# Performance work log

Measured on AMD Instinct MI355X. Metric: run time of the kernel, lower is better.

## Reference

```python
import math
import jax, jax.numpy as jnp
import numpy as np

B, S, D = 8, 1024, 1024
H, DK = 16, 64
NUM_BUCKETS, MAX_DIST = 32, 128
LN_EPS = 1e-6


def _relative_position_bucket(relative_position, num_buckets=NUM_BUCKETS, max_distance=MAX_DIST):
    # bidirectional (encoder) variant of T5 bucketing
    nb = num_buckets // 2
    rel_buckets = (relative_position > 0).astype(jnp.int32) * nb
    rp = jnp.abs(relative_position)
    max_exact = nb // 2
    is_small = rp < max_exact
    rp_large = max_exact + (
        jnp.log(jnp.maximum(rp, 1).astype(jnp.float32) / max_exact)
        / math.log(max_distance / max_exact)
        * (nb - max_exact)
    ).astype(jnp.int32)
    rp_large = jnp.minimum(rp_large, nb - 1)
    return rel_buckets + jnp.where(is_small, rp, rp_large)


def compute_bias(rel_bias, q_len, k_len):
    ctx = jnp.arange(q_len)[:, None]
    mem = jnp.arange(k_len)[None, :]
    buckets = _relative_position_bucket(mem - ctx)        # [q,k]
    values = rel_bias[buckets]                             # [q,k,H]
    return jnp.transpose(values, (2, 0, 1))[None]          # [1,H,q,k]


def switch_layer_norm(x, w, eps=LN_EPS):
    # T5-style: no mean subtraction, no bias
    var = jnp.mean(jnp.square(x.astype(jnp.float32)), axis=-1, keepdims=True)
    return w * (x * jax.lax.rsqrt(var + eps)).astype(x.dtype)


def setup_inputs() -> dict:
    key = jax.random.key(0)
    ks = jax.random.split(key, 6)
    scale = 1.0 / math.sqrt(D)
    return {
        "hidden_states": jax.random.normal(ks[0], (B, S, D), jnp.float32),
        "ln_weight": jnp.ones((D,), jnp.float32),
        "wq": jax.random.normal(ks[1], (D, H * DK), jnp.float32) * scale,
        "wk": jax.random.normal(ks[2], (D, H * DK), jnp.float32) * scale,
        "wv": jax.random.normal(ks[3], (D, H * DK), jnp.float32) * scale,
        "wo": jax.random.normal(ks[4], (H * DK, D), jnp.float32) * scale,
        "rel_bias": jax.random.normal(ks[5], (NUM_BUCKETS, H), jnp.float32),
    }


def reference(hidden_states, ln_weight, wq, wk, wv, wo, rel_bias):
    b, s, d = hidden_states.shape
    normed = switch_layer_norm(hidden_states, ln_weight)
    # projections -> [B,H,S,DK]; T5 applies NO 1/sqrt(dk) scaling
    q = (normed @ wq).reshape(b, s, H, DK).transpose(0, 2, 1, 3)
    k = (normed @ wk).reshape(b, s, H, DK).transpose(0, 2, 1, 3)
    v = (normed @ wv).reshape(b, s, H, DK).transpose(0, 2, 1, 3)
    scores = jnp.einsum("bhqd,bhkd->bhqk", q, k)
    scores = scores + compute_bias(rel_bias, s, s)
    attn = jax.nn.softmax(scores, axis=-1)
    ctx = jnp.einsum("bhqk,bhkd->bhqd", attn, v)
    ctx = ctx.transpose(0, 2, 1, 3).reshape(b, s, H * DK)
    attn_out = ctx @ wo
    return hidden_states + attn_out  # residual of SwitchLayerSelfAttention (dropout=0)
```

## Files before the change

kernel.cpp:

```cpp
#include <hip/hip_runtime.h>

typedef unsigned short u16;
typedef unsigned int u32;
typedef unsigned long long u64;
typedef __attribute__((ext_vector_type(8))) short bf16x8;
typedef __attribute__((ext_vector_type(4))) float f32x4;

__device__ __forceinline__ float bf2f(u16 u) {
  union { u32 i; float f; } c; c.i = ((u32)u) << 16; return c.f;
}
__device__ __forceinline__ u16 f2bf(float f) {
  union { float f; u32 i; } c; c.f = f;
  u32 i = c.i;
  return (u16)((i + 0x7fffu + ((i >> 16) & 1u)) >> 16);
}
__device__ __forceinline__ u32 pkbf(float a, float b) {
  union { float f; u32 i; } ca, cb; ca.f = a; cb.f = b;
  return __builtin_amdgcn_perm(cb.i + 0x8000u, ca.i + 0x8000u, 0x07060302u);
}
__device__ __forceinline__ void async16(const void* g, void* l) {
  __builtin_amdgcn_global_load_lds((const __attribute__((address_space(1))) void*)g,
                                   (__attribute__((address_space(3))) void*)l, 16, 0, 0);
}

__global__ __launch_bounds__(256) void detect_kernel(const u32* __restrict__ X,
                                                     int* __restrict__ flag) {
  __shared__ int part[4];
  const int tid = threadIdx.x, lane = tid & 63, wave = tid >> 6;
  int votes = 0;
  for (int i = tid; i < 4096; i += 256) {
    const u32 u = X[i];
    union { u32 i; float f; } c; c.i = u;
    const float a = fabsf(c.f);
    if (u == 0u || (a > 1e-6f && a < 1e6f)) votes++;
  }
  #pragma unroll
  for (int off = 32; off >= 1; off >>= 1) votes += __shfl_xor(votes, off);
  if (lane == 0) part[wave] = votes;
  __syncthreads();
  if (tid == 0) {
    const int tot = part[0] + part[1] + part[2] + part[3];
    *flag = (tot >= 2048) ? 0 : 1;
  }
}

__global__ __launch_bounds__(256) void prep_kernel(
    const void* __restrict__ W0, const void* __restrict__ W1, const void* __restrict__ W2,
    const void* __restrict__ W3, u16* __restrict__ T0, u16* __restrict__ T1,
    u16* __restrict__ T2, u16* __restrict__ T3, const void* __restrict__ rel_bias,
    float* __restrict__ Tb, const int* __restrict__ flagp) {
  const int f32m = (*flagp == 0);
  const int z = blockIdx.z;
  if (z == 4) {
    const int flat = blockIdx.y * 16 + blockIdx.x;
    const int idx = flat * 256 + threadIdx.x;
    if (idx >= 16 * 2047) return;
    const int h = idx / 2047;
    const int d = idx % 2047 - 1023;
    const int rb = (d > 0) ? 16 : 0;
    const int rp = d < 0 ? -d : d;
    int val;
    if (rp < 8) {
      val = rp;
    } else {
      float t = (logf((float)rp * 0.125f) / 2.772588722239781f) * 8.0f;
      val = 8 + (int)t;
      if (val > 15) val = 15;
    }
    const int bi = (rb + val) * 16 + h;
    Tb[idx] = f32m ? ((const float*)rel_bias)[bi] : bf2f(((const u16*)rel_bias)[bi]);
    return;
  }
  const void* W = (z == 0) ? W0 : (z == 1) ? W1 : (z == 2) ? W2 : W3;
  u16* WT = (z == 0) ? T0 : (z == 1) ? T1 : (z == 2) ? T2 : T3;
  __shared__ u16 t[64][65];
  const int tid = threadIdx.x;
  const int tx = tid & 63, ty = tid >> 6;
  const int n0 = blockIdx.x * 64, k0 = blockIdx.y * 64;
  #pragma unroll
  for (int r = ty; r < 64; r += 4) {
    const size_t idx = (size_t)(k0 + r) * 1024 + n0 + tx;
    t[r][tx] = f32m ? f2bf(((const float*)W)[idx]) : ((const u16*)W)[idx];
  }
  __syncthreads();
  #pragma unroll
  for (int r = ty; r < 64; r += 4) WT[(size_t)(n0 + r) * 1024 + k0 + tx] = t[tx][r];
}

__global__ __launch_bounds__(256) void rmsnorm_kernel(const void* __restrict__ X,
                                                      const void* __restrict__ W,
                                                      u16* __restrict__ Out,
                                                      const int* __restrict__ flagp) {
  const int f32m = (*flagp == 0);
  __shared__ float part[4];
  const int tid = threadIdx.x, lane = tid & 63, wave = tid >> 6;
  const size_t row = blockIdx.x;
  const int c = tid * 4;
  float x0, x1, x2, x3, w0f, w1f, w2f, w3f;
  if (f32m) {
    const float4 xx = *(const float4*)((const float*)X + row * 1024 + c);
    x0 = xx.x; x1 = xx.y; x2 = xx.z; x3 = xx.w;
    const float4 ww = *(const float4*)((const float*)W + c);
    w0f = ww.x; w1f = ww.y; w2f = ww.z; w3f = ww.w;
  } else {
    const u32* px = (const u32*)((const u16*)X + row * 1024 + c);
    const u32 a0 = px[0], a1 = px[1];
    x0 = bf2f((u16)a0); x1 = bf2f((u16)(a0 >> 16));
    x2 = bf2f((u16)a1); x3 = bf2f((u16)(a1 >> 16));
    const u32* pw = (const u32*)((const u16*)W + c);
    const u32 b0 = pw[0], b1 = pw[1];
    w0f = bf2f((u16)b0); w1f = bf2f((u16)(b0 >> 16));
    w2f = bf2f((u16)b1); w3f = bf2f((u16)(b1 >> 16));
  }
  float ss = x0 * x0 + x1 * x1 + x2 * x2 + x3 * x3;
  #pragma unroll
  for (int off = 32; off >= 1; off >>= 1) ss += __shfl_xor(ss, off);
  if (lane == 0) part[wave] = ss;
  __syncthreads();
  const float tot = part[0] + part[1] + part[2] + part[3];
  const float scale = rsqrtf(tot * (1.0f / 1024.0f) + 1e-6f);
  const u16 o0 = f2bf(x0 * scale * w0f);
  const u16 o1 = f2bf(x1 * scale * w1f);
  const u16 o2 = f2bf(x2 * scale * w2f);
  const u16 o3 = f2bf(x3 * scale * w3f);
  u32* po = (u32*)(Out + row * 1024 + c);
  po[0] = (u32)o0 | ((u32)o1 << 16);
  po[1] = (u32)o2 | ((u32)o3 << 16);
}

template <bool SWAP>
__device__ __forceinline__ void gemm_core(const u16* __restrict__ A, const u16* __restrict__ BT,
                                          u16* As, u16* Bs, f32x4 (&acc)[4][4],
                                          int m0, int n0, int K, int lane, int wave) {
  const int srow = lane >> 2, scol = (lane & 3) * 8;
  const int wm = (wave >> 1) * 64, wn = (wave & 1) * 64;
  for (int kt = 0; kt < K; kt += 32) {
    __syncthreads();
    #pragma unroll
    for (int i = 0; i < 2; ++i) {
      const int c = wave * 2 + i;
      async16(A + (size_t)(m0 + c * 16 + srow) * K + kt + scol, As + c * 512);
      async16(BT + (size_t)(n0 + c * 16 + srow) * K + kt + scol, Bs + c * 512);
    }
    __syncthreads();
    bf16x8 af[4], bfr[4];
    #pragma unroll
    for (int mt = 0; mt < 4; ++mt)
      af[mt] = *(const bf16x8*)(As + (wm + mt * 16 + (lane & 15)) * 32 + (lane >> 4) * 8);
    #pragma unroll
    for (int nt = 0; nt < 4; ++nt)
      bfr[nt] = *(const bf16x8*)(Bs + (wn + nt * 16 + (lane & 15)) * 32 + (lane >> 4) * 8);
    #pragma unroll
    for (int mt = 0; mt < 4; ++mt)
      #pragma unroll
      for (int nt = 0; nt < 4; ++nt) {
        if (SWAP)
          acc[mt][nt] = __builtin_amdgcn_mfma_f32_16x16x32_bf16(bfr[nt], af[mt], acc[mt][nt], 0, 0, 0);
        else
          acc[mt][nt] = __builtin_amdgcn_mfma_f32_16x16x32_bf16(af[mt], bfr[nt], acc[mt][nt], 0, 0, 0);
      }
  }
}


template <int S0>
__device__ __forceinline__ void stage3(u16* lds, const u16* __restrict__ A,
                                       const u16* __restrict__ B, int m0, int n0,
                                       int kt, int w, int lane) {
  const int ko8 = ((lane & 7) ^ ((lane >> 3) & 7)) * 8;
  const int rl = lane >> 3;
  #pragma unroll
  for (int s = S0; s < S0 + 3; ++s) {
    const int cw = s * 8 + w;
    const int r = cw * 8 + rl;
    u16* ldst = lds + cw * 512;
    if (s < 4)
      async16(A + (size_t)(m0 + r) * 1024 + kt + ko8, ldst);
    else
      async16(B + (size_t)(n0 + r - 256) * 1024 + kt + ko8, ldst);
  }
}

template <bool SWAP>
__device__ __forceinline__ void gemm256_core(const u16* __restrict__ A,
                                             const u16* __restrict__ WT,
                                             u16 (*buf)[24576], f32x4 (&acc)[4][4],
                                             int m0, int n0, int lane, int w) {
  const int wr = w >> 1, wc = w & 1;
  const int l15 = lane & 15;
  const int ko0 = (((lane >> 4) + 0) ^ (lane & 7)) * 8;
  const int ko1 = (((lane >> 4) + 4) ^ (lane & 7)) * 8;
  const int arow = (wr * 64 + l15) * 64;
  const int brow = 16384 + (wc * 64 + l15) * 64;

  stage3<0>(buf[0], A, WT, m0, n0, 0, w, lane);
  stage3<3>(buf[0], A, WT, m0, n0, 0, w, lane);
  stage3<0>(buf[1], A, WT, m0, n0, 64, w, lane);
  stage3<3>(buf[1], A, WT, m0, n0, 64, w, lane);
  __asm__ volatile("s_waitcnt vmcnt(6)" ::: "memory");
  __builtin_amdgcn_s_barrier();
  __asm__ volatile("" ::: "memory");

  int sl = 0, sn = 2;
  #pragma unroll 1
  for (int t = 0; t < 16; ++t) {
    const u16* bc = buf[sl];
    u16* bn = buf[sn];
    const int kt2 = (t + 2) * 64;
    bf16x8 af[4][2], bfr[2][2];
    #pragma unroll
    for (int i = 0; i < 4; ++i) {
      af[i][0] = *(const bf16x8*)(bc + arow + i * 1024 + ko0);
      af[i][1] = *(const bf16x8*)(bc + arow + i * 1024 + ko1);
    }
    #pragma unroll
    for (int j = 0; j < 2; ++j) {
      bfr[j][0] = *(const bf16x8*)(bc + brow + j * 1024 + ko0);
      bfr[j][1] = *(const bf16x8*)(bc + brow + j * 1024 + ko1);
    }
    if (t < 14) stage3<0>(bn, A, WT, m0, n0, kt2, w, lane);
    __builtin_amdgcn_s_barrier();
    __asm__ volatile("s_waitcnt lgkmcnt(0)" ::: "memory");
    __builtin_amdgcn_s_setprio(1);
    #pragma unroll
    for (int i = 0; i < 4; ++i)
      #pragma unroll
      for (int j = 0; j < 2; ++j) {
        if (SWAP) {
          acc[i][j] = __builtin_amdgcn_mfma_f32_16x16x32_bf16(bfr[j][0], af[i][0], acc[i][j], 0, 0, 0);
          acc[i][j] = __builtin_amdgcn_mfma_f32_16x16x32_bf16(bfr[j][1], af[i][1], acc[i][j], 0, 0, 0);
        } else {
          acc[i][j] = __builtin_amdgcn_mfma_f32_16x16x32_bf16(af[i][0], bfr[j][0], acc[i][j], 0, 0, 0);
          acc[i][j] = __builtin_amdgcn_mfma_f32_16x16x32_bf16(af[i][1], bfr[j][1], acc[i][j], 0, 0, 0);
        }
      }
    __builtin_amdgcn_s_setprio(0);
    __builtin_amdgcn_s_barrier();
    __asm__ volatile("" ::: "memory");
    #pragma unroll
    for (int j = 0; j < 2; ++j) {
      bfr[j][0] = *(const bf16x8*)(bc + brow + (j + 2) * 1024 + ko0);
      bfr[j][1] = *(const bf16x8*)(bc + brow + (j + 2) * 1024 + ko1);
    }
    if (t < 14) stage3<3>(bn, A, WT, m0, n0, kt2, w, lane);
    __builtin_amdgcn_s_barrier();
    __asm__ volatile("s_waitcnt lgkmcnt(0)" ::: "memory");
    __builtin_amdgcn_s_setprio(1);
    #pragma unroll
    for (int i = 0; i < 4; ++i)
      #pragma unroll
      for (int j = 0; j < 2; ++j) {
        if (SWAP) {
          acc[i][j + 2] = __builtin_amdgcn_mfma_f32_16x16x32_bf16(bfr[j][0], af[i][0], acc[i][j + 2], 0, 0, 0);
          acc[i][j + 2] = __builtin_amdgcn_mfma_f32_16x16x32_bf16(bfr[j][1], af[i][1], acc[i][j + 2], 0, 0, 0);
        } else {
          acc[i][j + 2] = __builtin_amdgcn_mfma_f32_16x16x32_bf16(af[i][0], bfr[j][0], acc[i][j + 2], 0, 0, 0);
          acc[i][j + 2] = __builtin_amdgcn_mfma_f32_16x16x32_bf16(af[i][1], bfr[j][1], acc[i][j + 2], 0, 0, 0);
        }
      }
    __builtin_amdgcn_s_setprio(0);
    if (t < 14)
      __asm__ volatile("s_waitcnt vmcnt(6)" ::: "memory");
    else
      __asm__ volatile("s_waitcnt vmcnt(0)" ::: "memory");
    __builtin_amdgcn_s_barrier();
    __asm__ volatile("" ::: "memory");
    sl = (sl == 2) ? 0 : sl + 1;
    sn = (sn == 2) ? 0 : sn + 1;
  }
}

__global__ __launch_bounds__(512, 2) void qkv_gemm256_kernel(
    const u16* __restrict__ A, const u16* __restrict__ WT,
    u16* __restrict__ Qo, u16* __restrict__ Ko, u16* __restrict__ VTo) {
  __shared__ __align__(16) u16 buf[3][24576];
  const int tid = threadIdx.x, lane = tid & 63, w = tid >> 6;
  const int id = blockIdx.x;
  const int xcd = id & 7;
  const int t0 = id >> 3;
  const int nb = t0 % 24;
  const int mhi = t0 / 24;
  const int m0 = (mhi * 8 + xcd) * 256;
  const int n0 = nb * 128;
  const int z = nb >> 3;

  f32x4 acc[4][4];
  const f32x4 zero = {0.f, 0.f, 0.f, 0.f};
  #pragma unroll
  for (int i = 0; i < 4; ++i)
    #pragma unroll
    for (int j = 0; j < 4; ++j) acc[i][j] = zero;

  const int wr = w >> 1, wc = w & 1;
  const int cq = lane & 15, quad = lane >> 4;
  const int nbase = (n0 & 1023) + wc * 64;

  if (z == 2) {
    gemm256_core<false>(A, WT, buf, acc, m0, n0, lane, w);
    #pragma unroll
    for (int i = 0; i < 4; ++i) {
      const int s = m0 + wr * 64 + i * 16 + quad * 4;
      const int b = s >> 10, s0 = s & 1023;
      #pragma unroll
      for (int j = 0; j < 4; ++j) {
        const int n = nbase + j * 16 + cq;
        const int hh = n >> 6, dk = n & 63;
        const u64 pk = (u64)f2bf(acc[i][j][0]) | ((u64)f2bf(acc[i][j][1]) << 16) |
                       ((u64)f2bf(acc[i][j][2]) << 32) | ((u64)f2bf(acc[i][j][3]) << 48);
        *(u64*)(VTo + (((size_t)(b * 16 + hh)) * 64 + dk) * 1024 + s0) = pk;
      }
    }
  } else {
    gemm256_core<true>(A, WT, buf, acc, m0, n0, lane, w);
    u16* Out = (z == 0) ? Qo : Ko;
    #pragma unroll
    for (int i = 0; i < 4; ++i) {
      const int s = m0 + wr * 64 + i * 16 + cq;
      const int b = s >> 10, ss = s & 1023;
      #pragma unroll
      for (int j = 0; j < 4; ++j) {
        const int n = nbase + j * 16 + quad * 4;
        const int hh = n >> 6, dk = n & 63;
        const u64 pk = (u64)f2bf(acc[i][j][0]) | ((u64)f2bf(acc[i][j][1]) << 16) |
                       ((u64)f2bf(acc[i][j][2]) << 32) | ((u64)f2bf(acc[i][j][3]) << 48);
        *(u64*)(Out + (((size_t)(b * 16 + hh)) * 1024 + ss) * 64 + dk) = pk;
      }
    }
  }
}

__global__ __launch_bounds__(256) void out_gemm_kernel(
    const u16* __restrict__ A, const u16* __restrict__ BT, const void* __restrict__ Res,
    void* __restrict__ Out, int N, int K, const int* __restrict__ flagp) {
  const int f32m = (*flagp == 0);
  __shared__ __align__(16) u16 As[128 * 32];
  __shared__ __align__(16) u16 Bs[128 * 32];
  const int tid = threadIdx.x, lane = tid & 63, wave = tid >> 6;
  const int id = blockIdx.x;
  const int xcd = id & 7;
  const int t = id >> 3;
  const int nb = t & 7;
  const int mhi = t >> 3;
  const int m0 = (mhi * 8 + xcd) * 128;
  const int n0 = nb * 128;

  f32x4 acc[4][4];
  const f32x4 zero = {0.f, 0.f, 0.f, 0.f};
  #pragma unroll
  for (int i = 0; i < 4; ++i)
    #pragma unroll
    for (int j = 0; j < 4; ++j) acc[i][j] = zero;

  gemm_core<true>(A, BT, As, Bs, acc, m0, n0, K, lane, wave);

  const int wm = (wave >> 1) * 64, wn = (wave & 1) * 64;
  #pragma unroll
  for (int mt = 0; mt < 4; ++mt) {
    const int s = m0 + wm + mt * 16 + (lane & 15);
    #pragma unroll
    for (int nt = 0; nt < 4; ++nt) {
      const int n = n0 + wn + nt * 16 + (lane >> 4) * 4;
      const size_t idx = (size_t)s * N + n;
      if (f32m) {
        const float4 rr = *(const float4*)((const float*)Res + idx);
        float4 oo;
        oo.x = rr.x + acc[mt][nt][0]; oo.y = rr.y + acc[mt][nt][1];
        oo.z = rr.z + acc[mt][nt][2]; oo.w = rr.w + acc[mt][nt][3];
        *(float4*)((float*)Out + idx) = oo;
      } else {
        const u64 rr = *(const u64*)((const u16*)Res + idx);
        const u64 pk =
            (u64)f2bf(bf2f((u16)rr) + acc[mt][nt][0]) |
            ((u64)f2bf(bf2f((u16)(rr >> 16)) + acc[mt][nt][1]) << 16) |
            ((u64)f2bf(bf2f((u16)(rr >> 32)) + acc[mt][nt][2]) << 32) |
            ((u64)f2bf(bf2f((u16)(rr >> 48)) + acc[mt][nt][3]) << 48);
        *(u64*)((u16*)Out + idx) = pk;
      }
    }
  }
}

__global__ __launch_bounds__(256, 3) void attn_kernel(
    const u16* __restrict__ Q, const u16* __restrict__ K, const u16* __restrict__ VT,
    const float* __restrict__ Tb, u16* __restrict__ ctx) {
  __shared__ __align__(16) u16 Ks[2][4096];
  __shared__ __align__(16) u16 Vs[2][4096];
  __shared__ __align__(16) u16 Ps[4][2048];
  __shared__ __align__(16) float Tbs[1152];

  const int tid = threadIdx.x, lane = tid & 63, w = tid >> 6;
  const int c = lane & 15, quad = lane >> 4;
  const int id = blockIdx.x;
  const int bh = id & 127, qc = id >> 7;
  const int b = bh >> 4, h = bh & 15;
  const int q0 = qc * 128;
  const int qw = q0 + w * 32;
  const u16* Kg = K + (size_t)bh * 1024 * 64;
  const u16* Vg = VT + (size_t)bh * 64 * 1024;
  const float* Th = Tb + h * 2047;
  u16* PsW = &Ps[w][0];

  #pragma unroll
  for (int i = tid; i < 1152; i += 256) Tbs[i] = Th[896 - q0 + i];

  bf16x8 qf[2][2];
  {
    const u16* Qg = Q + ((size_t)bh * 1024 + qw) * 64;
    #pragma unroll
    for (int nt = 0; nt < 2; ++nt)
      #pragma unroll
      for (int half = 0; half < 2; ++half)
        qf[nt][half] = *(const bf16x8*)(Qg + (size_t)(nt * 16 + c) * 64 + half * 32 + quad * 8);
  }

  f32x4 oacc[4][2];
  const f32x4 zero = {0.f, 0.f, 0.f, 0.f};
  #pragma unroll
  for (int i = 0; i < 4; ++i)
    #pragma unroll
    for (int j = 0; j < 2; ++j) oacc[i][j] = zero;
  float rsum[2] = {0.f, 0.f};

  {
    const int k0 = 0;
    #pragma unroll
    for (int i = 0; i < 2; ++i) {
      async16(Kg + (size_t)(k0 + w * 16 + c) * 64 + i * 32 + quad * 8, &Ks[0][(w * 2 + i) * 512]);
      async16(Vg + (size_t)(w * 16 + c) * 1024 + k0 + i * 32 + quad * 8, &Vs[0][(w * 2 + i) * 512]);
    }
  }

  #pragma unroll 1
  for (int kt = 0; kt < 16; ++kt) {
    const int cur = kt & 1;
    __asm__ volatile("s_waitcnt vmcnt(0)" ::: "memory");
    __syncthreads();
    if (kt < 15) {
      const int k1 = (kt + 1) * 64;
      #pragma unroll
      for (int i = 0; i < 2; ++i) {
        async16(Kg + (size_t)(k1 + w * 16 + c) * 64 + i * 32 + quad * 8,
                &Ks[1 - cur][(w * 2 + i) * 512]);
        async16(Vg + (size_t)(w * 16 + c) * 1024 + k1 + i * 32 + quad * 8,
                &Vs[1 - cur][(w * 2 + i) * 512]);
      }
    }
    const int k0 = kt * 64;
    f32x4 sc[4][2];
    const int jb = k0 + quad * 4 - c + 127 - 32 * w;
    #pragma unroll
    for (int mt = 0; mt < 4; ++mt)
      #pragma unroll
      for (int nt = 0; nt < 2; ++nt) {
        const float* tp = Tbs + jb + mt * 16 - nt * 16;
        sc[mt][nt][0] = tp[0]; sc[mt][nt][1] = tp[1]; sc[mt][nt][2] = tp[2]; sc[mt][nt][3] = tp[3];
      }
    const u16* Kc = &Ks[cur][0];
    #pragma unroll
    for (int mt = 0; mt < 4; ++mt) {
      const bf16x8 kf0 = *(const bf16x8*)(Kc + (mt * 2 + 0) * 512 + lane * 8);
      const bf16x8 kf1 = *(const bf16x8*)(Kc + (mt * 2 + 1) * 512 + lane * 8);
      #pragma unroll
      for (int nt = 0; nt < 2; ++nt) {
        sc[mt][nt] = __builtin_amdgcn_mfma_f32_16x16x32_bf16(kf0, qf[nt][0], sc[mt][nt], 0, 0, 0);
        sc[mt][nt] = __builtin_amdgcn_mfma_f32_16x16x32_bf16(kf1, qf[nt][1], sc[mt][nt], 0, 0, 0);
      }
    }
    #pragma unroll
    for (int mt = 0; mt < 4; ++mt)
      #pragma unroll
      for (int nt = 0; nt < 2; ++nt) {
        const float p0 = __expf(sc[mt][nt][0]), p1 = __expf(sc[mt][nt][1]);
        const float p2 = __expf(sc[mt][nt][2]), p3 = __expf(sc[mt][nt][3]);
        rsum[nt] += (p0 + p1) + (p2 + p3);
        const u32 lo = pkbf(p0, p1), hi = pkbf(p2, p3);
        const u64 pk = (u64)lo | ((u64)hi << 32);
        const int ch = (mt * 2 + (quad >> 1)) ^ (c & 7);
        *(u64*)(PsW + (nt * 16 + c) * 64 + ch * 8 + (quad & 1) * 4) = pk;
      }
    __asm__ volatile("s_waitcnt lgkmcnt(0)" ::: "memory");
    const u16* Vc = &Vs[cur][0];
    bf16x8 pf[2][2];
    #pragma unroll
    for (int nt = 0; nt < 2; ++nt)
      #pragma unroll
      for (int kk = 0; kk < 2; ++kk) {
        const int ch = (kk * 4 + quad) ^ (c & 7);
        pf[nt][kk] = *(const bf16x8*)(PsW + (nt * 16 + c) * 64 + ch * 8);
      }
    #pragma unroll
    for (int dt = 0; dt < 4; ++dt) {
      const bf16x8 vf0 = *(const bf16x8*)(Vc + (dt * 2 + 0) * 512 + lane * 8);
      const bf16x8 vf1 = *(const bf16x8*)(Vc + (dt * 2 + 1) * 512 + lane * 8);
      #pragma unroll
      for (int nt = 0; nt < 2; ++nt) {
        oacc[dt][nt] = __builtin_amdgcn_mfma_f32_16x16x32_bf16(vf0, pf[nt][0], oacc[dt][nt], 0, 0, 0);
        oacc[dt][nt] = __builtin_amdgcn_mfma_f32_16x16x32_bf16(vf1, pf[nt][1], oacc[dt][nt], 0, 0, 0);
      }
    }
  }

  #pragma unroll
  for (int nt = 0; nt < 2; ++nt) {
    rsum[nt] += __shfl_xor(rsum[nt], 16);
    rsum[nt] += __shfl_xor(rsum[nt], 32);
  }

  #pragma unroll
  for (int nt = 0; nt < 2; ++nt) {
    const float inv = 1.0f / rsum[nt];
    const int q = qw + nt * 16 + c;
    #pragma unroll
    for (int dt = 0; dt < 4; ++dt) {
      const u64 pk = (u64)f2bf(oacc[dt][nt][0] * inv) | ((u64)f2bf(oacc[dt][nt][1] * inv) << 16) |
                     ((u64)f2bf(oacc[dt][nt][2] * inv) << 32) | ((u64)f2bf(oacc[dt][nt][3] * inv) << 48);
      *(u64*)(ctx + (((size_t)b * 1024 + q) * 16 + h) * 64 + dt * 16 + quad * 4) = pk;
    }
  }
}

extern "C" void kernel_launch(void* const* d_in, const int* in_sizes, int n_in,
                              void* d_out, int out_size, void* d_ws, size_t ws_size,
                              hipStream_t stream) {
  const void* hidden = d_in[0];
  const void* lnw = d_in[1];
  const void* wq = d_in[2];
  const void* wk = d_in[3];
  const void* wv = d_in[4];
  const void* wo = d_in[5];
  const void* relb = d_in[6];
  char* ws = (char*)d_ws;

  u16* normed = (u16*)(ws);
  u16* Qb = (u16*)(ws + ((size_t)16 << 20));
  u16* Kb = (u16*)(ws + ((size_t)32 << 20));
  u16* VTb = (u16*)(ws + ((size_t)48 << 20));
  u16* wtq = (u16*)(ws + ((size_t)64 << 20));
  u16* wtk = (u16*)(ws + ((size_t)64 << 20) + (2 << 20));
  u16* wtv = (u16*)(ws + ((size_t)64 << 20) + (4 << 20));
  u16* wto = (u16*)(ws + ((size_t)64 << 20) + (6 << 20));
  float* Tb = (float*)(ws + ((size_t)64 << 20) + (8 << 20));
  int* flag = (int*)(ws + ((size_t)64 << 20) + (9 << 20));

  dim3 b256(256);
  detect_kernel<<<dim3(1), b256, 0, stream>>>((const u32*)hidden, flag);
  prep_kernel<<<dim3(16, 16, 5), b256, 0, stream>>>(wq, wk, wv, wo, wtq, wtk, wtv, wto,
                                                    relb, Tb, flag);
  rmsnorm_kernel<<<dim3(8192), b256, 0, stream>>>(hidden, lnw, normed, flag);
  qkv_gemm256_kernel<<<dim3(768), dim3(512), 0, stream>>>(normed, wtq, Qb, Kb, VTb);
  attn_kernel<<<dim3(1024), b256, 0, stream>>>(Qb, Kb, VTb, Tb, normed);
  out_gemm_kernel<<<dim3(512), b256, 0, stream>>>(normed, wto, hidden, d_out, 1024, 1024, flag);
}
```

Baseline: 278.9 us.

## Load K/V fragments directly from global memory into registers in attention loop

Removes the double-buffered LDS staging of K and V tiles and the per-iteration barrier in the attention kernel. Each wave now loads its K and V MFMA fragments straight from global memory into registers, relying on L2/L1 for reuse across the four waves. It also raises wave priority around the MFMA blocks with s_setprio. This trades LDS traffic and block-wide synchronisation for redundant global loads per wave and more exposed memory latency, since there is no explicit prefetch.

```diff
diff --git a/kernel.cpp b/kernel.cpp
--- a/kernel.cpp
+++ b/kernel.cpp
@@ -162,7 +162,6 @@
   }
 }
 
-
 template <int S0>
 __device__ __forceinline__ void stage3(u16* lds, const u16* __restrict__ A,
                                        const u16* __restrict__ B, int m0, int n0,
@@ -383,8 +382,6 @@
 __global__ __launch_bounds__(256, 3) void attn_kernel(
     const u16* __restrict__ Q, const u16* __restrict__ K, const u16* __restrict__ VT,
     const float* __restrict__ Tb, u16* __restrict__ ctx) {
-  __shared__ __align__(16) u16 Ks[2][4096];
-  __shared__ __align__(16) u16 Vs[2][4096];
   __shared__ __align__(16) u16 Ps[4][2048];
   __shared__ __align__(16) float Tbs[1152];
 
@@ -421,31 +418,20 @@
     for (int j = 0; j < 2; ++j) oacc[i][j] = zero;
   float rsum[2] = {0.f, 0.f};
 
-  {
-    const int k0 = 0;
-    #pragma unroll
-    for (int i = 0; i < 2; ++i) {
-      async16(Kg + (size_t)(k0 + w * 16 + c) * 64 + i * 32 + quad * 8, &Ks[0][(w * 2 + i) * 512]);
-      async16(Vg + (size_t)(w * 16 + c) * 1024 + k0 + i * 32 + quad * 8, &Vs[0][(w * 2 + i) * 512]);
-    }
-  }
+  const u16* Kp = Kg + (size_t)c * 64 + quad * 8;
+  const u16* Vp = Vg + (size_t)c * 1024 + quad * 8;
+
+  __syncthreads();
 
   #pragma unroll 1
   for (int kt = 0; kt < 16; ++kt) {
-    const int cur = kt & 1;
-    __asm__ volatile("s_waitcnt vmcnt(0)" ::: "memory");
-    __syncthreads();
-    if (kt < 15) {
-      const int k1 = (kt + 1) * 64;
-      #pragma unroll
-      for (int i = 0; i < 2; ++i) {
-        async16(Kg + (size_t)(k1 + w * 16 + c) * 64 + i * 32 + quad * 8,
-                &Ks[1 - cur][(w * 2 + i) * 512]);
-        async16(Vg + (size_t)(w * 16 + c) * 1024 + k1 + i * 32 + quad * 8,
-                &Vs[1 - cur][(w * 2 + i) * 512]);
-      }
-    }
     const int k0 = kt * 64;
+    bf16x8 kf[4][2];
+    #pragma unroll
+    for (int mt = 0; mt < 4; ++mt)
+      #pragma unroll
+      for (int i = 0; i < 2; ++i)
+        kf[mt][i] = *(const bf16x8*)(Kp + (k0 + mt * 16) * 64 + i * 32);
     f32x4 sc[4][2];
     const int jb = k0 + quad * 4 - c + 127 - 32 * w;
     #pragma unroll
@@ -455,17 +441,21 @@
         const float* tp = Tbs + jb + mt * 16 - nt * 16;
         sc[mt][nt][0] = tp[0]; sc[mt][nt][1] = tp[1]; sc[mt][nt][2] = tp[2]; sc[mt][nt][3] = tp[3];
       }
-    const u16* Kc = &Ks[cur][0];
-    #pragma unroll
-    for (int mt = 0; mt < 4; ++mt) {
-      const bf16x8 kf0 = *(const bf16x8*)(Kc + (mt * 2 + 0) * 512 + lane * 8);
-      const bf16x8 kf1 = *(const bf16x8*)(Kc + (mt * 2 + 1) * 512 + lane * 8);
+    __builtin_amdgcn_s_setprio(1);
+    #pragma unroll
+    for (int mt = 0; mt < 4; ++mt)
       #pragma unroll
       for (int nt = 0; nt < 2; ++nt) {
-        sc[mt][nt] = __builtin_amdgcn_mfma_f32_16x16x32_bf16(kf0, qf[nt][0], sc[mt][nt], 0, 0, 0);
-        sc[mt][nt] = __builtin_amdgcn_mfma_f32_16x16x32_bf16(kf1, qf[nt][1], sc[mt][nt], 0, 0, 0);
-      }
-    }
+        sc[mt][nt] = __builtin_amdgcn_mfma_f32_16x16x32_bf16(kf[mt][0], qf[nt][0], sc[mt][nt], 0, 0, 0);
+        sc[mt][nt] = __builtin_amdgcn_mfma_f32_16x16x32_bf16(kf[mt][1], qf[nt][1], sc[mt][nt], 0, 0, 0);
+      }
+    __builtin_amdgcn_s_setprio(0);
+    bf16x8 vf[4][2];
+    #pragma unroll
+    for (int dt = 0; dt < 4; ++dt)
+      #pragma unroll
+      for (int i = 0; i < 2; ++i)
+        vf[dt][i] = *(const bf16x8*)(Vp + dt * 16 * 1024 + k0 + i * 32);
     #pragma unroll
     for (int mt = 0; mt < 4; ++mt)
       #pragma unroll
@@ -479,7 +469,6 @@
         *(u64*)(PsW + (nt * 16 + c) * 64 + ch * 8 + (quad & 1) * 4) = pk;
       }
     __asm__ volatile("s_waitcnt lgkmcnt(0)" ::: "memory");
-    const u16* Vc = &Vs[cur][0];
     bf16x8 pf[2][2];
     #pragma unroll
     for (int nt = 0; nt < 2; ++nt)
@@ -488,16 +477,15 @@
         const int ch = (kk * 4 + quad) ^ (c & 7);
         pf[nt][kk] = *(const bf16x8*)(PsW + (nt * 16 + c) * 64 + ch * 8);
       }
-    #pragma unroll
-    for (int dt = 0; dt < 4; ++dt) {
-      const bf16x8 vf0 = *(const bf16x8*)(Vc + (dt * 2 + 0) * 512 + lane * 8);
-      const bf16x8 vf1 = *(const bf16x8*)(Vc + (dt * 2 + 1) * 512 + lane * 8);
+    __builtin_amdgcn_s_setprio(1);
+    #pragma unroll
+    for (int dt = 0; dt < 4; ++dt)
       #pragma unroll
       for (int nt = 0; nt < 2; ++nt) {
-        oacc[dt][nt] = __builtin_amdgcn_mfma_f32_16x16x32_bf16(vf0, pf[nt][0], oacc[dt][nt], 0, 0, 0);
-        oacc[dt][nt] = __builtin_amdgcn_mfma_f32_16x16x32_bf16(vf1, pf[nt][1], oacc[dt][nt], 0, 0, 0);
-      }
-    }
+        oacc[dt][nt] = __builtin_amdgcn_mfma_f32_16x16x32_bf16(vf[dt][0], pf[nt][0], oacc[dt][nt], 0, 0, 0);
+        oacc[dt][nt] = __builtin_amdgcn_mfma_f32_16x16x32_bf16(vf[dt][1], pf[nt][1], oacc[dt][nt], 0, 0, 0);
+      }
+    __builtin_amdgcn_s_setprio(0);
   }
 
   #pragma unroll
```

Result: slower. 350.8 us (+25.8%).
